# Kernel tuning notes

Hardware: AMD Instinct MI355X
Metric: run time of the kernel (lower is better)

Reference implementation:

```python
import jax, jax.numpy as jnp
import numpy as np

N_NODES = 50000
N_EDGES = 640000
IN_SIZE = 512
HID1 = 128


def setup_inputs() -> dict:
    key = jax.random.key(0)
    ks = jax.random.split(key, 7)
    x = jax.random.normal(ks[0], (N_NODES, IN_SIZE), dtype=jnp.float32)
    edge_index = jax.random.randint(ks[1], (2, N_EDGES), 0, N_NODES, dtype=jnp.int64)
    # Linear params stored as (in, out) so y = x @ W + b (equiv to torch x @ W.T + b)
    s_enc = 1.0 / np.sqrt(IN_SIZE)
    s_dec = 1.0 / np.sqrt(HID1)
    W_enc = jax.random.uniform(ks[2], (IN_SIZE, HID1), jnp.float32, -s_enc, s_enc)
    b_enc = jax.random.uniform(ks[3], (HID1,), jnp.float32, -s_enc, s_enc)
    W_dec = jax.random.uniform(ks[4], (HID1, IN_SIZE), jnp.float32, -s_dec, s_dec)
    b_dec = jax.random.uniform(ks[5], (IN_SIZE,), jnp.float32, -s_dec, s_dec)
    gcn_bias = jnp.zeros((HID1,), dtype=jnp.float32)  # reset_parameters zeroes it
    return {"x": x, "W_enc": W_enc, "b_enc": b_enc, "W_dec": W_dec,
            "b_dec": b_dec, "gcn_bias": gcn_bias, "edge_index": edge_index}


def gcn_conv(h, edge_index, bias):
    # GCNConv with lin.weight frozen to identity (in==out), so lin is a no-op.
    N = h.shape[0]
    loops = jnp.arange(N, dtype=edge_index.dtype)
    row = jnp.concatenate([edge_index[0], loops])  # source nodes (x_j)
    col = jnp.concatenate([edge_index[1], loops])  # target nodes (aggregation)
    deg = jax.ops.segment_sum(jnp.ones_like(col, dtype=h.dtype), col, num_segments=N)
    dinv = jnp.where(deg > 0, jax.lax.rsqrt(deg), jnp.zeros_like(deg))
    norm = dinv[row] * dinv[col]              # [E+N]
    msg = norm[:, None] * h[row]              # gather + scale, [E+N, HID1]
    out = jax.ops.segment_sum(msg, col, num_segments=N)  # scatter-add
    return out + bias


def reference(x, W_enc, b_enc, W_dec, b_dec, gcn_bias, edge_index):
    encoded = jax.nn.relu(x @ W_enc + b_enc)          # [N, HID1]
    messaged = gcn_conv(encoded, edge_index, gcn_bias)
    decoded = jax.nn.sigmoid(messaged @ W_dec + b_dec)  # [N, IN_SIZE]
    return decoded
```

## Files before the change

### kernel.cpp

```cpp
#include <hip/hip_runtime.h>
#include <math.h>

#define NNODES 50000
#define NEDGES 640000
#define INSZ 512
#define HID 128
#define NBLK ((NNODES + 255) / 256)

typedef short s16x8 __attribute__((ext_vector_type(8)));
typedef float f32x4 __attribute__((ext_vector_type(4)));

static __device__ inline short f2bf(float f) {
    __bf16 b = (__bf16)f;
    return __builtin_bit_cast(short, b);
}

__global__ __launch_bounds__(256) void prep_wenc(const float* __restrict__ W,
                                                 short* __restrict__ WT) {
    int t = blockIdx.x * 256 + threadIdx.x;
    if (t < INSZ * HID) {
        int n = t & (HID - 1);
        int k = t >> 7;
        WT[n * INSZ + k] = f2bf(W[t]);
    }
}
__global__ __launch_bounds__(256) void prep_wdec(const float* __restrict__ W,
                                                 short* __restrict__ WT) {
    int t = blockIdx.x * 256 + threadIdx.x;
    if (t < HID * INSZ) {
        int n = t & (INSZ - 1);
        int k = t >> 9;
        WT[n * HID + k] = f2bf(W[t]);
    }
}

__global__ __launch_bounds__(256) void count_kernel(const int* __restrict__ col,
                                                    int* __restrict__ counts) {
    int e = blockIdx.x * blockDim.x + threadIdx.x;
    if (e < NEDGES) atomicAdd(&counts[col[e]], 1);
}

__global__ __launch_bounds__(256) void partial_kernel(const int* __restrict__ counts,
                                                      int* __restrict__ blocksums) {
    int i = blockIdx.x * 256 + threadIdx.x;
    int v = (i < NNODES) ? counts[i] : 0;
#pragma unroll
    for (int off = 32; off; off >>= 1) v += __shfl_down(v, off, 64);
    __shared__ int ws[4];
    if ((threadIdx.x & 63) == 0) ws[threadIdx.x >> 6] = v;
    __syncthreads();
    if (threadIdx.x == 0) blocksums[blockIdx.x] = ws[0] + ws[1] + ws[2] + ws[3];
}

__global__ __launch_bounds__(256) void scan_blocks(const int* __restrict__ blocksums,
                                                   int* __restrict__ blockoffs) {
    __shared__ int s[256];
    const int t = threadIdx.x;
    s[t] = (t < NBLK) ? blocksums[t] : 0;
    __syncthreads();
    for (int off = 1; off < 256; off <<= 1) {
        int u = (t >= off) ? s[t - off] : 0;
        __syncthreads();
        s[t] += u;
        __syncthreads();
    }
    blockoffs[t] = (t == 0) ? 0 : s[t - 1];
}

__global__ __launch_bounds__(256) void scan_final(const int* __restrict__ counts,
                                                  const int* __restrict__ blockoffs,
                                                  int* __restrict__ starts,
                                                  int* __restrict__ cursor,
                                                  float* __restrict__ dinv) {
    __shared__ int s[256];
    const int t = threadIdx.x;
    const int i = blockIdx.x * 256 + t;
    int v = (i < NNODES) ? counts[i] : 0;
    s[t] = v;
    __syncthreads();
    for (int off = 1; off < 256; off <<= 1) {
        int u = (t >= off) ? s[t - off] : 0;
        __syncthreads();
        s[t] += u;
        __syncthreads();
    }
    int excl = ((t == 0) ? 0 : s[t - 1]) + blockoffs[blockIdx.x];
    if (i < NNODES) {
        starts[i] = excl;
        cursor[i] = excl;
        dinv[i] = rsqrtf((float)v + 1.0f);
        if (i == NNODES - 1) starts[NNODES] = excl + v;
    }
}

__global__ __launch_bounds__(256) void scatter_kernel(const int* __restrict__ erow,
                                                      const int* __restrict__ ecol,
                                                      int* __restrict__ cursor,
                                                      int* __restrict__ csr_row) {
    int e = blockIdx.x * blockDim.x + threadIdx.x;
    if (e < NEDGES) {
        int pos = atomicAdd(&cursor[ecol[e]], 1);
        csr_row[pos] = erow[e];
    }
}

#define XPAD 72
__global__ __launch_bounds__(256) void encoder_mfma(const float* __restrict__ x,
                                                    const short* __restrict__ WT,
                                                    const float* __restrict__ b,
                                                    float* __restrict__ h) {
    __shared__ short xs[2][64 * XPAD];
    const int t    = threadIdx.x;
    const int lane = t & 63;
    const int wv   = t >> 6;
    const int r16  = lane & 15;
    const int kg   = lane >> 4;
    const int mbase = blockIdx.x * 64;
    const int nb    = wv * 32;

    const float4* sp[4];
    int sdst[4];
#pragma unroll
    for (int j = 0; j < 4; ++j) {
        int c = j * 256 + t;
        int row = c >> 4, c4 = c & 15;
        int gr = mbase + row; if (gr >= NNODES) gr = NNODES - 1;
        sp[j]   = (const float4*)x + (size_t)gr * (INSZ / 4) + c4;
        sdst[j] = row * XPAD + c4 * 4;
    }

    f32x4 acc[4][2] = {};
    float4 rcur[4], rnxt[4];
#pragma unroll
    for (int j = 0; j < 4; ++j) rcur[j] = sp[j][0];

    int cur = 0;
    for (int ks = 0; ks < 8; ++ks) {
        if (ks < 7) {
#pragma unroll
            for (int j = 0; j < 4; ++j) rnxt[j] = sp[j][(ks + 1) * 16];
        }
#pragma unroll
        for (int j = 0; j < 4; ++j) {
            short4 w;
            w.x = f2bf(rcur[j].x); w.y = f2bf(rcur[j].y);
            w.z = f2bf(rcur[j].z); w.w = f2bf(rcur[j].w);
            *(short4*)&xs[cur][sdst[j]] = w;
        }
        __syncthreads();
#pragma unroll
        for (int kk = 0; kk < 2; ++kk) {
            s16x8 a[4], bb[2];
#pragma unroll
            for (int mt = 0; mt < 4; ++mt)
                a[mt] = *(const s16x8*)&xs[cur][(mt * 16 + r16) * XPAD + kk * 32 + kg * 8];
#pragma unroll
            for (int nt = 0; nt < 2; ++nt)
                bb[nt] = *(const s16x8*)(WT + (size_t)(nb + nt * 16 + r16) * INSZ + ks * 64 + kk * 32 + kg * 8);
#pragma unroll
            for (int mt = 0; mt < 4; ++mt)
#pragma unroll
                for (int nt = 0; nt < 2; ++nt)
                    acc[mt][nt] = __builtin_amdgcn_mfma_f32_16x16x32_bf16(a[mt], bb[nt], acc[mt][nt], 0, 0, 0);
        }
#pragma unroll
        for (int j = 0; j < 4; ++j) rcur[j] = rnxt[j];
        cur ^= 1;
        __syncthreads();
    }

    const int ro = kg * 4;
#pragma unroll
    for (int mt = 0; mt < 4; ++mt) {
        const int row0 = mbase + mt * 16 + ro;
#pragma unroll
        for (int nt = 0; nt < 2; ++nt) {
            const int col = nb + nt * 16 + r16;
            const float bj = b[col];
#pragma unroll
            for (int v = 0; v < 4; ++v) {
                int rr = row0 + v;
                if (rr < NNODES)
                    h[(size_t)rr * HID + col] = fmaxf(acc[mt][nt][v] + bj, 0.0f);
            }
        }
    }
}

__global__ __launch_bounds__(256) void aggregate_csr_kernel(const int* __restrict__ starts,
                                                            const int* __restrict__ csr_row,
                                                            const float* __restrict__ dinv,
                                                            const float* __restrict__ h,
                                                            float* __restrict__ agg) {
    const int node = (blockIdx.x * 256 + threadIdx.x) >> 5;
    const int l32  = threadIdx.x & 31;
    if (node >= NNODES) return;
    const float dc = dinv[node];
    const int s0 = starts[node], s1 = starts[node + 1];
    const float4* hp = (const float4*)h;

    float4 acc = hp[(size_t)node * 32 + l32];
    const float sc = dc * dc;
    acc.x *= sc; acc.y *= sc; acc.z *= sc; acc.w *= sc;

    int i = s0;
    for (; i + 3 < s1; i += 4) {
        int r0 = csr_row[i], r1 = csr_row[i + 1], r2 = csr_row[i + 2], r3 = csr_row[i + 3];
        float n0 = dinv[r0] * dc, n1 = dinv[r1] * dc, n2 = dinv[r2] * dc, n3 = dinv[r3] * dc;
        float4 h0 = hp[(size_t)r0 * 32 + l32];
        float4 h1 = hp[(size_t)r1 * 32 + l32];
        float4 h2 = hp[(size_t)r2 * 32 + l32];
        float4 h3 = hp[(size_t)r3 * 32 + l32];
        acc.x = fmaf(n0, h0.x, acc.x); acc.y = fmaf(n0, h0.y, acc.y);
        acc.z = fmaf(n0, h0.z, acc.z); acc.w = fmaf(n0, h0.w, acc.w);
        acc.x = fmaf(n1, h1.x, acc.x); acc.y = fmaf(n1, h1.y, acc.y);
        acc.z = fmaf(n1, h1.z, acc.z); acc.w = fmaf(n1, h1.w, acc.w);
        acc.x = fmaf(n2, h2.x, acc.x); acc.y = fmaf(n2, h2.y, acc.y);
        acc.z = fmaf(n2, h2.z, acc.z); acc.w = fmaf(n2, h2.w, acc.w);
        acc.x = fmaf(n3, h3.x, acc.x); acc.y = fmaf(n3, h3.y, acc.y);
        acc.z = fmaf(n3, h3.z, acc.z); acc.w = fmaf(n3, h3.w, acc.w);
    }
    for (; i < s1; ++i) {
        int r = csr_row[i];
        float nrm = dinv[r] * dc;
        float4 hv = hp[(size_t)r * 32 + l32];
        acc.x = fmaf(nrm, hv.x, acc.x); acc.y = fmaf(nrm, hv.y, acc.y);
        acc.z = fmaf(nrm, hv.z, acc.z); acc.w = fmaf(nrm, hv.w, acc.w);
    }
    ((float4*)agg)[(size_t)node * 32 + l32] = acc;
}

#define APAD 136
#define EPAD 68
__global__ __launch_bounds__(512) void decoder_mfma(const float* __restrict__ agg,
                                                    const float* __restrict__ gb,
                                                    const short* __restrict__ WT,
                                                    const float* __restrict__ b,
                                                    float* __restrict__ out) {
    __shared__ short as_lds[64 * APAD];
    __shared__ float ep[8][16 * EPAD];
    const int t    = threadIdx.x;
    const int lane = t & 63;
    const int wv   = t >> 6;
    const int r16  = lane & 15;
    const int kg   = lane >> 4;
    const int mbase = blockIdx.x * 64;
    const int nwb   = wv * 64;

    {
        const int row = t >> 3;
        const int f0  = (t & 7) * 16;
        int gr = mbase + row; if (gr >= NNODES) gr = NNODES - 1;
        const float4* src4 = (const float4*)(agg + (size_t)gr * HID + f0);
        const float4* g4   = (const float4*)(gb + f0);
        short4* d4 = (short4*)(as_lds + row * APAD + f0);
#pragma unroll
        for (int j = 0; j < 4; ++j) {
            float4 u = src4[j], g = g4[j];
            short4 w;
            w.x = f2bf(u.x + g.x); w.y = f2bf(u.y + g.y);
            w.z = f2bf(u.z + g.z); w.w = f2bf(u.w + g.w);
            d4[j] = w;
        }
    }
    __syncthreads();

    f32x4 acc[4][4] = {};
#pragma unroll
    for (int ks = 0; ks < 4; ++ks) {
        s16x8 a[4], bb[4];
#pragma unroll
        for (int mt = 0; mt < 4; ++mt)
            a[mt] = *(const s16x8*)&as_lds[(mt * 16 + r16) * APAD + ks * 32 + kg * 8];
#pragma unroll
        for (int nt = 0; nt < 4; ++nt)
            bb[nt] = *(const s16x8*)(WT + (size_t)(nwb + nt * 16 + r16) * HID + ks * 32 + kg * 8);
#pragma unroll
        for (int mt = 0; mt < 4; ++mt)
#pragma unroll
            for (int nt = 0; nt < 4; ++nt)
                acc[mt][nt] = __builtin_amdgcn_mfma_f32_16x16x32_bf16(a[mt], bb[nt], acc[mt][nt], 0, 0, 0);
    }

    float bj[4];
#pragma unroll
    for (int nt = 0; nt < 4; ++nt) bj[nt] = b[nwb + nt * 16 + r16];

    float* eps = ep[wv];
#pragma unroll
    for (int mt = 0; mt < 4; ++mt) {
#pragma unroll
        for (int nt = 0; nt < 4; ++nt)
#pragma unroll
            for (int v = 0; v < 4; ++v) {
                float z = acc[mt][nt][v] + bj[nt];
                eps[(kg * 4 + v) * EPAD + nt * 16 + r16] = 1.0f / (1.0f + __expf(-z));
            }
#pragma unroll
        for (int pass = 0; pass < 4; ++pass) {
            const int lr = pass * 4 + kg;
            float4 vv = *(const float4*)&eps[lr * EPAD + r16 * 4];
            const int rr = mbase + mt * 16 + lr;
            if (rr < NNODES)
                *(float4*)&out[(size_t)rr * INSZ + nwb + r16 * 4] = vv;
        }
    }
}

extern "C" void kernel_launch(void* const* d_in, const int* in_sizes, int n_in,
                              void* d_out, int out_size, void* d_ws, size_t ws_size,
                              hipStream_t stream) {
    const float* x        = (const float*)d_in[0];
    const float* W_enc    = (const float*)d_in[1];
    const float* b_enc    = (const float*)d_in[2];
    const float* W_dec    = (const float*)d_in[3];
    const float* b_dec    = (const float*)d_in[4];
    const float* gcn_bias = (const float*)d_in[5];
    const int*   edge     = (const int*)d_in[6];
    const int*   erow = edge;
    const int*   ecol = edge + NEDGES;

    float* out = (float*)d_out;
    float* agg   = (float*)d_ws;
    float* dinv  = agg + (size_t)NNODES * HID;
    short* wdecT = (short*)(dinv + NNODES);
    float* h         = out;
    int*   csr_row   = (int*)(out + (size_t)NNODES * HID);
    int*   starts    = csr_row + NEDGES;
    int*   counts    = starts + NNODES + 1;
    int*   cursor    = counts + NNODES;
    int*   blocksums = cursor + NNODES;
    int*   blockoffs = blocksums + 256;
    short* wencT     = (short*)(blockoffs + 256);

    hipMemsetAsync(counts, 0, (size_t)NNODES * sizeof(int), stream);
    prep_wenc<<<(INSZ * HID + 255) / 256, 256, 0, stream>>>(W_enc, wencT);
    prep_wdec<<<(HID * INSZ + 255) / 256, 256, 0, stream>>>(W_dec, wdecT);
    count_kernel<<<(NEDGES + 255) / 256, 256, 0, stream>>>(ecol, counts);
    partial_kernel<<<NBLK, 256, 0, stream>>>(counts, blocksums);
    scan_blocks<<<1, 256, 0, stream>>>(blocksums, blockoffs);
    scan_final<<<NBLK, 256, 0, stream>>>(counts, blockoffs, starts, cursor, dinv);
    scatter_kernel<<<(NEDGES + 255) / 256, 256, 0, stream>>>(erow, ecol, cursor, csr_row);
    encoder_mfma<<<(NNODES + 63) / 64, 256, 0, stream>>>(x, wencT, b_enc, h);
    aggregate_csr_kernel<<<((size_t)NNODES * 32 + 255) / 256, 256, 0, stream>>>(starts, csr_row, dinv, h, agg);
    decoder_mfma<<<(NNODES + 63) / 64, 512, 0, stream>>>(agg, gcn_bias, wdecT, b_dec, out);
}
```

Measured before the change: 216.9 us.

## Stage whole 64x512 x tile in LDS before MFMA loop instead of double-buffering

The encoder now loads the block's entire 64-row by 512-column slice of x, converts it to bf16 and stores it in one LDS buffer with a single barrier, then runs all 16 k-steps of MFMA without further synchronisation. This replaces the 8-stage register-prefetch double-buffer, which needed two barriers per stage. The aim is to cut barrier overhead and issue wider 32-byte loads with 16-byte LDS stores. In exchange LDS use per block grows to about 66 KB, which can lower occupancy, and load latency is no longer overlapped with compute inside a block.

```diff
diff --git a/kernel.cpp b/kernel.cpp
--- a/kernel.cpp
+++ b/kernel.cpp
@@ -104,12 +104,12 @@
     }
 }
 
-#define XPAD 72
+#define XP 520
 __global__ __launch_bounds__(256) void encoder_mfma(const float* __restrict__ x,
                                                     const short* __restrict__ WT,
                                                     const float* __restrict__ b,
                                                     float* __restrict__ h) {
-    __shared__ short xs[2][64 * XPAD];
+    __shared__ short xs[64 * XP];
     const int t    = threadIdx.x;
     const int lane = t & 63;
     const int wv   = t >> 6;
@@ -118,55 +118,45 @@
     const int mbase = blockIdx.x * 64;
     const int nb    = wv * 32;
 
-    const float4* sp[4];
-    int sdst[4];
-#pragma unroll
-    for (int j = 0; j < 4; ++j) {
-        int c = j * 256 + t;
-        int row = c >> 4, c4 = c & 15;
-        int gr = mbase + row; if (gr >= NNODES) gr = NNODES - 1;
-        sp[j]   = (const float4*)x + (size_t)gr * (INSZ / 4) + c4;
-        sdst[j] = row * XPAD + c4 * 4;
-    }
+    for (int i = 0; i < 4; ++i) {
+        float4 u[4], v[4];
+#pragma unroll
+        for (int j = 0; j < 4; ++j) {
+            int p = (i * 4 + j) * 256 + t;
+            int row = p >> 6, c8 = p & 63;
+            int gr = mbase + row; if (gr >= NNODES) gr = NNODES - 1;
+            const float4* src = (const float4*)(x + (size_t)gr * INSZ + c8 * 8);
+            u[j] = src[0]; v[j] = src[1];
+        }
+#pragma unroll
+        for (int j = 0; j < 4; ++j) {
+            int p = (i * 4 + j) * 256 + t;
+            int row = p >> 6, c8 = p & 63;
+            s16x8 w;
+            w[0] = f2bf(u[j].x); w[1] = f2bf(u[j].y);
+            w[2] = f2bf(u[j].z); w[3] = f2bf(u[j].w);
+            w[4] = f2bf(v[j].x); w[5] = f2bf(v[j].y);
+            w[6] = f2bf(v[j].z); w[7] = f2bf(v[j].w);
+            *(s16x8*)&xs[row * XP + c8 * 8] = w;
+        }
+    }
+    __syncthreads();
 
     f32x4 acc[4][2] = {};
-    float4 rcur[4], rnxt[4];
-#pragma unroll
-    for (int j = 0; j < 4; ++j) rcur[j] = sp[j][0];
-
-    int cur = 0;
-    for (int ks = 0; ks < 8; ++ks) {
-        if (ks < 7) {
-#pragma unroll
-            for (int j = 0; j < 4; ++j) rnxt[j] = sp[j][(ks + 1) * 16];
-        }
-#pragma unroll
-        for (int j = 0; j < 4; ++j) {
-            short4 w;
-            w.x = f2bf(rcur[j].x); w.y = f2bf(rcur[j].y);
-            w.z = f2bf(rcur[j].z); w.w = f2bf(rcur[j].w);
-            *(short4*)&xs[cur][sdst[j]] = w;
-        }
-        __syncthreads();
-#pragma unroll
-        for (int kk = 0; kk < 2; ++kk) {
-            s16x8 a[4], bb[2];
-#pragma unroll
-            for (int mt = 0; mt < 4; ++mt)
-                a[mt] = *(const s16x8*)&xs[cur][(mt * 16 + r16) * XPAD + kk * 32 + kg * 8];
+#pragma unroll
+    for (int ks = 0; ks < 16; ++ks) {
+        s16x8 a[4], bb[2];
+#pragma unroll
+        for (int mt = 0; mt < 4; ++mt)
+            a[mt] = *(const s16x8*)&xs[(mt * 16 + r16) * XP + ks * 32 + kg * 8];
+#pragma unroll
+        for (int nt = 0; nt < 2; ++nt)
+            bb[nt] = *(const s16x8*)(WT + (size_t)(nb + nt * 16 + r16) * INSZ + ks * 32 + kg * 8);
+#pragma unroll
+        for (int mt = 0; mt < 4; ++mt)
 #pragma unroll
             for (int nt = 0; nt < 2; ++nt)
-                bb[nt] = *(const s16x8*)(WT + (size_t)(nb + nt * 16 + r16) * INSZ + ks * 64 + kk * 32 + kg * 8);
-#pragma unroll
-            for (int mt = 0; mt < 4; ++mt)
-#pragma unroll
-                for (int nt = 0; nt < 2; ++nt)
-                    acc[mt][nt] = __builtin_amdgcn_mfma_f32_16x16x32_bf16(a[mt], bb[nt], acc[mt][nt], 0, 0, 0);
-        }
-#pragma unroll
-        for (int j = 0; j < 4; ++j) rcur[j] = rnxt[j];
-        cur ^= 1;
-        __syncthreads();
+                acc[mt][nt] = __builtin_amdgcn_mfma_f32_16x16x32_bf16(a[mt], bb[nt], acc[mt][nt], 0, 0, 0);
     }
 
     const int ro = kg * 4;
```

Result: no change. 214.9 us (-1.0%).

## Store hidden activations in bf16 and stream encoder input via direct LDS loads

Applied to the files above, without the earlier changes.

Switches the encoder output h and aggregated features agg from fp32 to bf16 storage, halving the bytes gathered in the irregular aggregation and the bytes read by the decoder. The encoder now copies x tiles from global memory straight into LDS as fp32 with global_load_lds, does the bf16 conversion at fragment-read time, and sets a minimum-occupancy launch bound. Extra rounding of intermediates adds precision loss, and LDS use doubles because the tiles are kept in fp32.

```diff
diff --git a/kernel.cpp b/kernel.cpp
--- a/kernel.cpp
+++ b/kernel.cpp
@@ -13,6 +13,15 @@
 static __device__ inline short f2bf(float f) {
     __bf16 b = (__bf16)f;
     return __builtin_bit_cast(short, b);
+}
+static __device__ inline float bf2f(unsigned short u) {
+    unsigned int i = (unsigned int)u << 16;
+    return __builtin_bit_cast(float, i);
+}
+static __device__ inline void gload16(const float* g, float* l) {
+    __builtin_amdgcn_global_load_lds(
+        (const __attribute__((address_space(1))) void*)g,
+        (__attribute__((address_space(3))) void*)l, 16, 0, 0);
 }
 
 __global__ __launch_bounds__(256) void prep_wenc(const float* __restrict__ W,
@@ -104,12 +113,11 @@
     }
 }
 
-#define XPAD 72
-__global__ __launch_bounds__(256) void encoder_mfma(const float* __restrict__ x,
-                                                    const short* __restrict__ WT,
-                                                    const float* __restrict__ b,
-                                                    float* __restrict__ h) {
-    __shared__ short xs[2][64 * XPAD];
+__global__ __launch_bounds__(256, 4) void encoder_mfma(const float* __restrict__ x,
+                                                       const short* __restrict__ WT,
+                                                       const float* __restrict__ b,
+                                                       unsigned short* __restrict__ h) {
+    __shared__ float xs[2][64 * 64];
     const int t    = threadIdx.x;
     const int lane = t & 63;
     const int wv   = t >> 6;
@@ -118,42 +126,45 @@
     const int mbase = blockIdx.x * 64;
     const int nb    = wv * 32;
 
-    const float4* sp[4];
-    int sdst[4];
-#pragma unroll
-    for (int j = 0; j < 4; ++j) {
-        int c = j * 256 + t;
-        int row = c >> 4, c4 = c & 15;
-        int gr = mbase + row; if (gr >= NNODES) gr = NNODES - 1;
-        sp[j]   = (const float4*)x + (size_t)gr * (INSZ / 4) + c4;
-        sdst[j] = row * XPAD + c4 * 4;
-    }
+    const float* gsrc[4];
+#pragma unroll
+    for (int i = 0; i < 4; ++i) {
+        int gr = mbase + wv * 16 + i * 4 + (lane >> 4);
+        if (gr >= NNODES) gr = NNODES - 1;
+        gsrc[i] = x + (size_t)gr * INSZ + (lane & 15) * 4;
+    }
+    float* ldst[4];
+#pragma unroll
+    for (int i = 0; i < 4; ++i) ldst[i] = &xs[0][(wv * 16 + i * 4) * 64];
+    const int bufoff = 64 * 64;
+
+#pragma unroll
+    for (int i = 0; i < 4; ++i) gload16(gsrc[i], ldst[i]);
+    __syncthreads();
 
     f32x4 acc[4][2] = {};
-    float4 rcur[4], rnxt[4];
-#pragma unroll
-    for (int j = 0; j < 4; ++j) rcur[j] = sp[j][0];
-
-    int cur = 0;
+#pragma unroll
     for (int ks = 0; ks < 8; ++ks) {
+        const int cur = ks & 1;
         if (ks < 7) {
 #pragma unroll
-            for (int j = 0; j < 4; ++j) rnxt[j] = sp[j][(ks + 1) * 16];
-        }
-#pragma unroll
-        for (int j = 0; j < 4; ++j) {
-            short4 w;
-            w.x = f2bf(rcur[j].x); w.y = f2bf(rcur[j].y);
-            w.z = f2bf(rcur[j].z); w.w = f2bf(rcur[j].w);
-            *(short4*)&xs[cur][sdst[j]] = w;
-        }
-        __syncthreads();
+            for (int i = 0; i < 4; ++i)
+                gload16(gsrc[i] + (ks + 1) * 64, ldst[i] + (cur ? 0 : bufoff));
+        }
+        const float* xb = &xs[cur][0];
 #pragma unroll
         for (int kk = 0; kk < 2; ++kk) {
             s16x8 a[4], bb[2];
 #pragma unroll
-            for (int mt = 0; mt < 4; ++mt)
-                a[mt] = *(const s16x8*)&xs[cur][(mt * 16 + r16) * XPAD + kk * 32 + kg * 8];
+            for (int mt = 0; mt < 4; ++mt) {
+                const float* ap = xb + (mt * 16 + r16) * 64 + kk * 32 + kg * 8;
+                float4 f0 = *(const float4*)ap;
+                float4 f1 = *(const float4*)(ap + 4);
+                s16x8 w;
+                w[0] = f2bf(f0.x); w[1] = f2bf(f0.y); w[2] = f2bf(f0.z); w[3] = f2bf(f0.w);
+                w[4] = f2bf(f1.x); w[5] = f2bf(f1.y); w[6] = f2bf(f1.z); w[7] = f2bf(f1.w);
+                a[mt] = w;
+            }
 #pragma unroll
             for (int nt = 0; nt < 2; ++nt)
                 bb[nt] = *(const s16x8*)(WT + (size_t)(nb + nt * 16 + r16) * INSZ + ks * 64 + kk * 32 + kg * 8);
@@ -163,9 +174,6 @@
                 for (int nt = 0; nt < 2; ++nt)
                     acc[mt][nt] = __builtin_amdgcn_mfma_f32_16x16x32_bf16(a[mt], bb[nt], acc[mt][nt], 0, 0, 0);
         }
-#pragma unroll
-        for (int j = 0; j < 4; ++j) rcur[j] = rnxt[j];
-        cur ^= 1;
         __syncthreads();
     }
 
@@ -181,7 +189,7 @@
             for (int v = 0; v < 4; ++v) {
                 int rr = row0 + v;
                 if (rr < NNODES)
-                    h[(size_t)rr * HID + col] = fmaxf(acc[mt][nt][v] + bj, 0.0f);
+                    h[(size_t)rr * HID + col] = (unsigned short)f2bf(fmaxf(acc[mt][nt][v] + bj, 0.0f));
             }
         }
     }
@@ -190,49 +198,54 @@
 __global__ __launch_bounds__(256) void aggregate_csr_kernel(const int* __restrict__ starts,
                                                             const int* __restrict__ csr_row,
                                                             const float* __restrict__ dinv,
-                                                            const float* __restrict__ h,
-                                                            float* __restrict__ agg) {
+                                                            const unsigned short* __restrict__ h,
+                                                            unsigned short* __restrict__ agg) {
     const int node = (blockIdx.x * 256 + threadIdx.x) >> 5;
     const int l32  = threadIdx.x & 31;
     if (node >= NNODES) return;
     const float dc = dinv[node];
     const int s0 = starts[node], s1 = starts[node + 1];
-    const float4* hp = (const float4*)h;
-
-    float4 acc = hp[(size_t)node * 32 + l32];
+    const ushort4* hp = (const ushort4*)h;
+
+    ushort4 sv = hp[(size_t)node * 32 + l32];
     const float sc = dc * dc;
-    acc.x *= sc; acc.y *= sc; acc.z *= sc; acc.w *= sc;
+    float4 acc;
+    acc.x = bf2f(sv.x) * sc; acc.y = bf2f(sv.y) * sc;
+    acc.z = bf2f(sv.z) * sc; acc.w = bf2f(sv.w) * sc;
 
     int i = s0;
     for (; i + 3 < s1; i += 4) {
         int r0 = csr_row[i], r1 = csr_row[i + 1], r2 = csr_row[i + 2], r3 = csr_row[i + 3];
         float n0 = dinv[r0] * dc, n1 = dinv[r1] * dc, n2 = dinv[r2] * dc, n3 = dinv[r3] * dc;
-        float4 h0 = hp[(size_t)r0 * 32 + l32];
-        float4 h1 = hp[(size_t)r1 * 32 + l32];
-        float4 h2 = hp[(size_t)r2 * 32 + l32];
-        float4 h3 = hp[(size_t)r3 * 32 + l32];
-        acc.x = fmaf(n0, h0.x, acc.x); acc.y = fmaf(n0, h0.y, acc.y);
-        acc.z = fmaf(n0, h0.z, acc.z); acc.w = fmaf(n0, h0.w, acc.w);
-        acc.x = fmaf(n1, h1.x, acc.x); acc.y = fmaf(n1, h1.y, acc.y);
-        acc.z = fmaf(n1, h1.z, acc.z); acc.w = fmaf(n1, h1.w, acc.w);
-        acc.x = fmaf(n2, h2.x, acc.x); acc.y = fmaf(n2, h2.y, acc.y);
-        acc.z = fmaf(n2, h2.z, acc.z); acc.w = fmaf(n2, h2.w, acc.w);
-        acc.x = fmaf(n3, h3.x, acc.x); acc.y = fmaf(n3, h3.y, acc.y);
-        acc.z = fmaf(n3, h3.z, acc.z); acc.w = fmaf(n3, h3.w, acc.w);
+        ushort4 h0 = hp[(size_t)r0 * 32 + l32];
+        ushort4 h1 = hp[(size_t)r1 * 32 + l32];
+        ushort4 h2 = hp[(size_t)r2 * 32 + l32];
+        ushort4 h3 = hp[(size_t)r3 * 32 + l32];
+        acc.x = fmaf(n0, bf2f(h0.x), acc.x); acc.y = fmaf(n0, bf2f(h0.y), acc.y);
+        acc.z = fmaf(n0, bf2f(h0.z), acc.z); acc.w = fmaf(n0, bf2f(h0.w), acc.w);
+        acc.x = fmaf(n1, bf2f(h1.x), acc.x); acc.y = fmaf(n1, bf2f(h1.y), acc.y);
+        acc.z = fmaf(n1, bf2f(h1.z), acc.z); acc.w = fmaf(n1, bf2f(h1.w), acc.w);
+        acc.x = fmaf(n2, bf2f(h2.x), acc.x); acc.y = fmaf(n2, bf2f(h2.y), acc.y);
+        acc.z = fmaf(n2, bf2f(h2.z), acc.z); acc.w = fmaf(n2, bf2f(h2.w), acc.w);
+        acc.x = fmaf(n3, bf2f(h3.x), acc.x); acc.y = fmaf(n3, bf2f(h3.y), acc.y);
+        acc.z = fmaf(n3, bf2f(h3.z), acc.z); acc.w = fmaf(n3, bf2f(h3.w), acc.w);
     }
     for (; i < s1; ++i) {
         int r = csr_row[i];
         float nrm = dinv[r] * dc;
-        float4 hv = hp[(size_t)r * 32 + l32];
-        acc.x = fmaf(nrm, hv.x, acc.x); acc.y = fmaf(nrm, hv.y, acc.y);
-        acc.z = fmaf(nrm, hv.z, acc.z); acc.w = fmaf(nrm, hv.w, acc.w);
-    }
-    ((float4*)agg)[(size_t)node * 32 + l32] = acc;
+        ushort4 hv = hp[(size_t)r * 32 + l32];
+        acc.x = fmaf(nrm, bf2f(hv.x), acc.x); acc.y = fmaf(nrm, bf2f(hv.y), acc.y);
+        acc.z = fmaf(nrm, bf2f(hv.z), acc.z); acc.w = fmaf(nrm, bf2f(hv.w), acc.w);
+    }
+    ushort4 ov;
+    ov.x = (unsigned short)f2bf(acc.x); ov.y = (unsigned short)f2bf(acc.y);
+    ov.z = (unsigned short)f2bf(acc.z); ov.w = (unsigned short)f2bf(acc.w);
+    ((ushort4*)agg)[(size_t)node * 32 + l32] = ov;
 }
 
 #define APAD 136
 #define EPAD 68
-__global__ __launch_bounds__(512) void decoder_mfma(const float* __restrict__ agg,
+__global__ __launch_bounds__(512) void decoder_mfma(const unsigned short* __restrict__ agg,
                                                     const float* __restrict__ gb,
                                                     const short* __restrict__ WT,
                                                     const float* __restrict__ b,
@@ -251,15 +264,16 @@
         const int row = t >> 3;
         const int f0  = (t & 7) * 16;
         int gr = mbase + row; if (gr >= NNODES) gr = NNODES - 1;
-        const float4* src4 = (const float4*)(agg + (size_t)gr * HID + f0);
-        const float4* g4   = (const float4*)(gb + f0);
+        const ushort4* src4 = (const ushort4*)(agg + (size_t)gr * HID + f0);
+        const float4*  g4   = (const float4*)(gb + f0);
         short4* d4 = (short4*)(as_lds + row * APAD + f0);
 #pragma unroll
         for (int j = 0; j < 4; ++j) {
-            float4 u = src4[j], g = g4[j];
+            ushort4 u = src4[j];
+            float4 g = g4[j];
             short4 w;
-            w.x = f2bf(u.x + g.x); w.y = f2bf(u.y + g.y);
-            w.z = f2bf(u.z + g.z); w.w = f2bf(u.w + g.w);
+            w.x = f2bf(bf2f(u.x) + g.x); w.y = f2bf(bf2f(u.y) + g.y);
+            w.z = f2bf(bf2f(u.z) + g.z); w.w = f2bf(bf2f(u.w) + g.w);
             d4[j] = w;
         }
     }
@@ -321,10 +335,10 @@
     const int*   ecol = edge + NEDGES;
 
     float* out = (float*)d_out;
-    float* agg   = (float*)d_ws;
-    float* dinv  = agg + (size_t)NNODES * HID;
+    unsigned short* agg = (unsigned short*)d_ws;
+    float* dinv  = (float*)(agg + (size_t)NNODES * HID);
     short* wdecT = (short*)(dinv + NNODES);
-    float* h         = out;
+    unsigned short* h = (unsigned short*)out;
     int*   csr_row   = (int*)(out + (size_t)NNODES * HID);
     int*   starts    = csr_row + NEDGES;
     int*   counts    = starts + NNODES + 1;
```

Result: slower. 247.2 us (+13.9%).
